# Kernel optimization log

Hardware: AMD Instinct MI355X
Metric: run time of the kernel (lower is better)

## Reference

```python
import jax, jax.numpy as jnp
import numpy as np


def setup_inputs() -> dict:
    key = jax.random.key(0)
    ks = jax.random.split(key, 7)
    B, S, E, N, H = 2, 2048, 1024, 8, 4096
    scale = 0.02
    return {
        "x": jax.random.normal(ks[0], (B, S, E), dtype=jnp.float32),
        "Wr": jax.random.normal(ks[1], (E, N), dtype=jnp.float32) * scale,
        "br": jnp.zeros((N,), dtype=jnp.float32),
        "W1": jax.random.normal(ks[2], (N, E, H), dtype=jnp.float32) * scale,
        "b1": jnp.zeros((N, H), dtype=jnp.float32),
        "W2": jax.random.normal(ks[3], (N, H, E), dtype=jnp.float32) * scale,
        "b2": jnp.zeros((N, E), dtype=jnp.float32),
        "top_k": 2,
    }


def reference(x, Wr, br, W1, b1, W2, b2, top_k):
    # Router: logits [B,S,N], keep top-k, softmax over the kept entries.
    logits = jnp.einsum("bse,en->bsn", x, Wr) + br
    _, idx = jax.lax.top_k(logits, top_k)                      # [B,S,k]
    mask = jax.nn.one_hot(idx, logits.shape[-1], dtype=jnp.bool_).any(-2)  # [B,S,N]
    masked = jnp.where(mask, logits, -jnp.inf)
    weights = jax.nn.softmax(masked, axis=-1)                   # [B,S,N]

    # Dense all-experts FFN (faithful to original): every expert on every token.
    # hid: [B,S,N,H]
    hid = jax.nn.gelu(jnp.einsum("bse,neh->bsnh", x, W1) + b1, approximate=False)
    expert_out = jnp.einsum("bsnh,nhe->bsne", hid, W2) + b2    # [B,S,N,E]
    # dropout is identity in eval mode

    # Weighted combine over experts.
    return jnp.einsum("bsne,bsn->bse", expert_out, weights)
```

## Files before the change

kernel.cpp:

```cpp
#include <hip/hip_runtime.h>
#include <hip/hip_bf16.h>
#include <cmath>
#include <cstdint>


typedef unsigned short u16;
typedef __attribute__((ext_vector_type(8))) short bf16x8;
typedef __attribute__((ext_vector_type(4))) float f32x4;
typedef __attribute__((ext_vector_type(8))) unsigned short us8;
typedef __attribute__((ext_vector_type(4))) unsigned short us4;

#define TOKENS  4096
#define EDIM    1024
#define NEXP    8
#define HDIM    4096
#define MAXROWS 8192
#define ROWPAD  384
#define MAXTILES 40
#define RBLK    1024

#define MFMA16(va, vb, vc) __builtin_amdgcn_mfma_f32_16x16x32_bf16(va, vb, vc, 0, 0, 0)

__device__ __forceinline__ u16 f2bf(float f) {
  __hip_bfloat16 h = __float2bfloat16(f);
  return *reinterpret_cast<u16*>(&h);
}
__device__ __forceinline__ int clampk(int k) {
  return k < 1 ? 1 : (k > 8 ? 8 : k);
}
__device__ __forceinline__ void async16(void* lds, const void* g) {
  __builtin_amdgcn_global_load_lds((const __attribute__((address_space(1))) void*)g,
                                   (__attribute__((address_space(3))) void*)lds,
                                   16, 0, 0);
}
__device__ __forceinline__ float gelu_f(float v) {
  const float z = fabsf(v) * 0.70710678118654752f;
  const float t = __builtin_amdgcn_rcpf(fmaf(0.3275911f, z, 1.0f));
  const float p = t * fmaf(t, fmaf(t, fmaf(t, fmaf(t, 1.061405429f, -1.453152027f),
                                           1.421413741f), -0.284496736f), 0.254829592f);
  float er = 1.0f - p * __expf(-z * z);
  er = copysignf(er, v);
  return 0.5f * v * (1.0f + er);
}

__global__ void router_k(const float* __restrict__ x, const float* __restrict__ Wr,
                         const float* __restrict__ br, const int* __restrict__ topk_p,
                         int* __restrict__ sel_e, float* __restrict__ sel_w,
                         int* __restrict__ sel_lpos, int* __restrict__ hist_blk) {
  __shared__ int wsel[4][8];
  const int blk = blockIdx.x;
  const int tid = threadIdx.x;
  const int wv = tid >> 6, ln = tid & 63;
  const int t = blk * 4 + wv;
  const int k = clampk(topk_p[0]);
  float acc[NEXP];
#pragma unroll
  for (int n = 0; n < NEXP; ++n) acc[n] = 0.f;
  const float* xr = x + (size_t)t * EDIM;
  for (int ei = ln; ei < EDIM; ei += 64) {
    float xv = xr[ei];
    float4 w0 = *(const float4*)(Wr + ei * NEXP);
    float4 w1 = *(const float4*)(Wr + ei * NEXP + 4);
    acc[0] += xv * w0.x; acc[1] += xv * w0.y; acc[2] += xv * w0.z; acc[3] += xv * w0.w;
    acc[4] += xv * w1.x; acc[5] += xv * w1.y; acc[6] += xv * w1.z; acc[7] += xv * w1.w;
  }
#pragma unroll
  for (int s = 32; s > 0; s >>= 1) {
#pragma unroll
    for (int n = 0; n < NEXP; ++n) acc[n] += __shfl_down(acc[n], s);
  }
  if (ln == 0) {
    float logit[NEXP];
#pragma unroll
    for (int n = 0; n < NEXP; ++n) logit[n] = acc[n] + br[n];
    bool used[NEXP];
#pragma unroll
    for (int n = 0; n < NEXP; ++n) used[n] = false;
    int se[NEXP]; float sw[NEXP];
    for (int j = 0; j < k; ++j) {
      int bi = 0; float bv = -INFINITY;
      for (int n = 0; n < NEXP; ++n)
        if (!used[n] && logit[n] > bv) { bv = logit[n]; bi = n; }
      used[bi] = true; se[j] = bi; sw[j] = bv;
    }
    float mx = sw[0], sum = 0.f;
    for (int j = 0; j < k; ++j) { sw[j] = expf(sw[j] - mx); sum += sw[j]; }
    float inv = 1.f / sum;
    for (int j = 0; j < k; ++j) {
      sel_e[t * 8 + j] = se[j];
      sel_w[t * 8 + j] = sw[j] * inv;
      wsel[wv][j] = se[j];
    }
  }
  __syncthreads();
  if (tid == 0) {
    int h[NEXP];
#pragma unroll
    for (int e = 0; e < NEXP; ++e) h[e] = 0;
    for (int w = 0; w < 4; ++w)
      for (int j = 0; j < k; ++j) {
        int e = wsel[w][j];
        sel_lpos[(blk * 4 + w) * 8 + j] = h[e]++;
      }
#pragma unroll
    for (int e = 0; e < NEXP; ++e) hist_blk[blk * NEXP + e] = h[e];
  }
}

__global__ void scan_k(const int* __restrict__ hist_blk, int* __restrict__ counts,
                       int* __restrict__ offsets, int* __restrict__ blk_base,
                       int* __restrict__ tmap) {
  __shared__ int sc[NEXP][257];
  __shared__ int offs[NEXP];
  const int tid = threadIdx.x;
  int h[4][NEXP], part[NEXP];
#pragma unroll
  for (int e = 0; e < NEXP; ++e) part[e] = 0;
#pragma unroll
  for (int r = 0; r < 4; ++r) {
    const int row = tid * 4 + r;
#pragma unroll
    for (int e = 0; e < NEXP; ++e) { h[r][e] = hist_blk[row * NEXP + e]; part[e] += h[r][e]; }
  }
#pragma unroll
  for (int e = 0; e < NEXP; ++e) sc[e][tid] = part[e];
  __syncthreads();
  for (int d = 1; d < 256; d <<= 1) {
    int v[NEXP];
#pragma unroll
    for (int e = 0; e < NEXP; ++e) v[e] = (tid >= d) ? sc[e][tid - d] : 0;
    __syncthreads();
#pragma unroll
    for (int e = 0; e < NEXP; ++e) sc[e][tid] += v[e];
    __syncthreads();
  }
  if (tid == 0) {
    int s = 0;
    for (int e = 0; e < NEXP; ++e) {
      int tot = sc[e][255];
      offsets[e] = s; offs[e] = s; counts[e] = tot; s += tot;
    }
    int nt = 0;
    for (int e = 0; e < NEXP; ++e) {
      int nb = (counts[e] + 255) >> 8;
      for (int b = 0; b < nb && nt < MAXTILES; ++b) tmap[nt++] = (e << 16) | b;
    }
    for (; nt < MAXTILES; ++nt) tmap[nt] = -1;
  }
  __syncthreads();
#pragma unroll
  for (int e = 0; e < NEXP; ++e) {
    int run = offs[e] + sc[e][tid] - part[e];
#pragma unroll
    for (int r = 0; r < 4; ++r) {
      blk_base[(tid * 4 + r) * NEXP + e] = run;
      run += h[r][e];
    }
  }
}

__global__ void finalize_k(const int* __restrict__ sel_e, const int* __restrict__ sel_lpos,
                           const int* __restrict__ blk_base, const int* __restrict__ topk_p,
                           int* __restrict__ sel_pos, int* __restrict__ row_token) {
  const int k = clampk(topk_p[0]);
  const int i = blockIdx.x * 256 + threadIdx.x;
  if (i >= TOKENS * k) return;
  const int t = i / k, j = i - t * k;
  const int e = sel_e[t * 8 + j];
  const int pos = blk_base[(t >> 2) * NEXP + e] + sel_lpos[t * 8 + j];
  sel_pos[t * 8 + j] = pos;
  row_token[pos] = t;
}

__global__ void gather_cast_k(const float* __restrict__ x, const int* __restrict__ row_token,
                              const int* __restrict__ counts, u16* __restrict__ xg,
                              float* __restrict__ Y) {
  __shared__ int tot_s;
  if (threadIdx.x == 0) {
    int t = 0;
#pragma unroll
    for (int e = 0; e < NEXP; ++e) t += counts[e];
    tot_s = t;
  }
  const int row = blockIdx.x;
  const int i = threadIdx.x;
  if (row < MAXROWS) {
    float4 z = {0.f, 0.f, 0.f, 0.f};
    *(float4*)(Y + (size_t)row * EDIM + i * 4) = z;
  }
  __syncthreads();
  u16* dst = xg + (size_t)row * EDIM;
  if (row >= tot_s) {
    us4 z = {0, 0, 0, 0};
    *(us4*)(dst + i * 4) = z;
    return;
  }
  const float* src = x + (size_t)row_token[row] * EDIM;
  float4 v = *(const float4*)(src + i * 4);
  us4 o; o[0] = f2bf(v.x); o[1] = f2bf(v.y); o[2] = f2bf(v.z); o[3] = f2bf(v.w);
  *(us4*)(dst + i * 4) = o;
}

__global__ void transpose_k(const float* __restrict__ W1, const float* __restrict__ W2,
                            u16* __restrict__ W1t, u16* __restrict__ W2t,
                            int full, int h0c) {
  __shared__ __align__(16) u16 T[64][68];
  const int z = blockIdx.z;
  int mat, e, h0;
  if (full) { mat = z < 32 ? 0 : 1; int zz = mat ? z - 32 : z; e = zz >> 2; h0 = (zz & 3) * 1024; }
  else      { mat = z < 8 ? 0 : 1;  e = mat ? z - 8 : z;      h0 = h0c; }
  const size_t oes = full ? (size_t)HDIM * EDIM : (size_t)1024 * 1024;
  const float* in; size_t istride;
  if (mat == 0) { in = W1 + (size_t)e * EDIM * HDIM + h0;            istride = HDIM; }
  else          { in = W2 + (size_t)e * HDIM * EDIM + (size_t)h0 * EDIM; istride = EDIM; }
  const int r0 = blockIdx.y * 64, c0 = blockIdx.x * 64;
  const int tid = threadIdx.x;
#pragma unroll
  for (int it = 0; it < 4; ++it) {
    int cell = it * 256 + tid;
    int rl = cell >> 4, c4 = (cell & 15) * 4;
    float4 v = *(const float4*)(in + (size_t)(r0 + rl) * istride + c0 + c4);
    us4 o; o[0] = f2bf(v.x); o[1] = f2bf(v.y); o[2] = f2bf(v.z); o[3] = f2bf(v.w);
    *(us4*)&T[rl][c4] = o;
  }
  __syncthreads();
#pragma unroll
  for (int it = 0; it < 2; ++it) {
    int cell = it * 256 + tid;
    int cl = cell >> 3, r8 = (cell & 7) * 8;
    us8 o;
#pragma unroll
    for (int j = 0; j < 8; ++j) o[j] = T[r8 + j][cl];
    u16* out;
    if (mat == 0) {
      int orow = (full ? h0 : 0) + c0 + cl;
      out = W1t + (size_t)e * oes + (size_t)orow * 1024 + r0 + r8;
    } else {
      int ost = full ? HDIM : 1024;
      out = W2t + (size_t)e * oes + (size_t)(c0 + cl) * ost + (full ? h0 : 0) + r0 + r8;
    }
    *(us8*)out = o;
  }
}

template <int MODE>
__global__ __launch_bounds__(512, 2) void gemm256_k(
    const u16* __restrict__ A, int astride, int kblocks,
    const u16* __restrict__ Bt, size_t b_estride, int bstride,
    const float* __restrict__ bias, int bias_dim, int bias_col0, int bias_on,
    const int* __restrict__ counts, const int* __restrict__ offsets,
    const int* __restrict__ tmap, int NB,
    u16* __restrict__ hid, int hid_stride, float* __restrict__ Y) {
  __shared__ __align__(16) char lds_s[131072];
  const int bid = blockIdx.x;
  const int by  = blockIdx.y;
  const int tile = bid / NB;
  const int tv = tmap[tile];
  if (tv < 0) return;
  const int n0 = (bid - tile * NB) << 8;
  const int e = tv >> 16;
  const int m0 = (tv & 0xffff) << 8;
  const int cnt = counts[e], off_e = offsets[e];

  const int tid = threadIdx.x;
  const int wv = tid >> 6, ln = tid & 63;
  const int wm = wv >> 2, wn = wv & 3;

  const int trow = tid >> 3;
  const int swz  = (tid & 7) ^ (trow & 7);
  const size_t koff = (size_t)by * kblocks * 64;
  const u16* gA = A + (size_t)(off_e + m0 + trow) * astride + koff + swz * 8;
  const u16* gB = Bt + (size_t)e * b_estride + (size_t)(n0 + trow) * bstride + koff + swz * 8;
  const size_t a64 = (size_t)astride * 64;
  const size_t b64 = (size_t)bstride * 64;
  char* const lA = lds_s + wv * 1024;
  char* const lB = lds_s + 65536 + wv * 1024;

  auto stage = [&](int buf, int kt) {
    const u16* ga = gA + (size_t)kt * 64;
    const u16* gb = gB + (size_t)kt * 64;
    char* la = lA + (buf << 15);
    char* lb = lB + (buf << 15);
#pragma unroll
    for (int h = 0; h < 4; ++h) async16(la + h * 8192, ga + (size_t)h * a64);
#pragma unroll
    for (int h = 0; h < 4; ++h) async16(lb + h * 8192, gb + (size_t)h * b64);
  };

  const int r15 = ln & 15, quad = ln >> 4, rs = r15 & 7;
  const int a_k0 = (wm * 128 + r15) * 128 + (((quad    ) ^ rs) << 4);
  const int a_k1 = (wm * 128 + r15) * 128 + (((quad + 4) ^ rs) << 4);
  const int b_k0 = (wn *  64 + r15) * 128 + (((quad    ) ^ rs) << 4);
  const int b_k1 = (wn *  64 + r15) * 128 + (((quad + 4) ^ rs) << 4);

  f32x4 acc[8][4];
#pragma unroll
  for (int i = 0; i < 8; ++i)
#pragma unroll
    for (int j = 0; j < 4; ++j) acc[i][j] = (f32x4){0.f, 0.f, 0.f, 0.f};

  bf16x8 a0[4], a1[4], b0[4], b1[4];

  stage(0, 0);
  __syncthreads();

  for (int t = 0; t < kblocks; ++t) {
    const int cb = (t & 1) << 15;
    const char* cA = lds_s + cb;
    const char* cB = lds_s + 65536 + cb;

#pragma unroll
    for (int mi = 0; mi < 4; ++mi) {
      a0[mi] = *(const bf16x8*)(cA + a_k0 + mi * 2048);
      a1[mi] = *(const bf16x8*)(cA + a_k1 + mi * 2048);
    }
#pragma unroll
    for (int ni = 0; ni < 4; ++ni) {
      b0[ni] = *(const bf16x8*)(cB + b_k0 + ni * 2048);
      b1[ni] = *(const bf16x8*)(cB + b_k1 + ni * 2048);
    }
    if (t + 1 < kblocks) stage((t & 1) ^ 1, t + 1);

#pragma unroll
    for (int mi = 0; mi < 4; ++mi)
#pragma unroll
      for (int ni = 0; ni < 4; ++ni) {
        acc[mi][ni] = MFMA16(a0[mi], b0[ni], acc[mi][ni]);
        acc[mi][ni] = MFMA16(a1[mi], b1[ni], acc[mi][ni]);
      }

#pragma unroll
    for (int mi = 0; mi < 4; ++mi) {
      a0[mi] = *(const bf16x8*)(cA + a_k0 + (mi + 4) * 2048);
      a1[mi] = *(const bf16x8*)(cA + a_k1 + (mi + 4) * 2048);
    }
#pragma unroll
    for (int mi = 0; mi < 4; ++mi)
#pragma unroll
      for (int ni = 0; ni < 4; ++ni) {
        acc[mi + 4][ni] = MFMA16(a0[mi], b0[ni], acc[mi + 4][ni]);
        acc[mi + 4][ni] = MFMA16(a1[mi], b1[ni], acc[mi + 4][ni]);
      }
    __syncthreads();
  }

  const int col0 = n0 + wn * 64 + r15;
  float bv[4];
#pragma unroll
  for (int ni = 0; ni < 4; ++ni) {
    const float b = bias[(size_t)e * bias_dim + bias_col0 + col0 + ni * 16];
    bv[ni] = (MODE == 0) ? b : ((bias_on && by == 0) ? b : 0.f);
  }
#pragma unroll
  for (int mi = 0; mi < 8; ++mi) {
    const int mb = m0 + wm * 128 + mi * 16 + quad * 4;
#pragma unroll
    for (int ni = 0; ni < 4; ++ni) {
      const int nc = col0 + ni * 16;
#pragma unroll
      for (int r = 0; r < 4; ++r) {
        const int m = mb + r;
        if (m < cnt) {
          const float v = acc[mi][ni][r] + bv[ni];
          if (MODE == 0) {
            hid[(size_t)(off_e + m) * hid_stride + nc] = f2bf(gelu_f(v));
          } else {
            atomicAdd(&Y[(size_t)(off_e + m) * EDIM + nc], v);
          }
        }
      }
    }
  }
}

__global__ void combine_k(const float* __restrict__ Y, const int* __restrict__ sel_pos,
                          const float* __restrict__ sel_w, const int* __restrict__ topk_p,
                          float* __restrict__ out) {
  const int t = blockIdx.x;
  const int tid = threadIdx.x;
  const int k = clampk(topk_p[0]);
  float a0 = 0.f, a1 = 0.f, a2 = 0.f, a3 = 0.f;
  for (int j = 0; j < k; ++j) {
    const float w = sel_w[t * 8 + j];
    const size_t row = (size_t)sel_pos[t * 8 + j];
    const float4 v = *(const float4*)(Y + row * EDIM + tid * 4);
    a0 += w * v.x; a1 += w * v.y; a2 += w * v.z; a3 += w * v.w;
  }
  float4 o; o.x = a0; o.y = a1; o.z = a2; o.w = a3;
  *(float4*)(out + (size_t)t * EDIM + tid * 4) = o;
}

extern "C" void kernel_launch(void* const* d_in, const int* in_sizes, int n_in,
                              void* d_out, int out_size, void* d_ws, size_t ws_size,
                              hipStream_t stream) {
  const float* x   = (const float*)d_in[0];
  const float* Wr  = (const float*)d_in[1];
  const float* br  = (const float*)d_in[2];
  const float* W1  = (const float*)d_in[3];
  const float* b1  = (const float*)d_in[4];
  const float* W2  = (const float*)d_in[5];
  const float* b2  = (const float*)d_in[6];
  const int* topk  = (const int*)d_in[7];
  float* out = (float*)d_out;

  char* ws = (char*)d_ws;
  size_t o = 0;
  auto alloc = [&](size_t bytes) -> char* {
    char* p = ws + o; o += (bytes + 255) & ~(size_t)255; return p;
  };
  int*   counts    = (int*)alloc(NEXP * 4);
  int*   offsets   = (int*)alloc(NEXP * 4);
  int*   tmap      = (int*)alloc(MAXTILES * 4);
  int*   sel_e     = (int*)alloc((size_t)TOKENS * 8 * 4);
  int*   sel_pos   = (int*)alloc((size_t)TOKENS * 8 * 4);
  int*   sel_lpos  = (int*)alloc((size_t)TOKENS * 8 * 4);
  float* sel_w     = (float*)alloc((size_t)TOKENS * 8 * 4);
  int*   row_token = (int*)alloc((size_t)TOKENS * 8 * 4);
  int*   hist_blk  = (int*)alloc((size_t)RBLK * NEXP * 4);
  int*   blk_base  = (int*)alloc((size_t)RBLK * NEXP * 4);
  u16*   xg        = (u16*)alloc((size_t)(MAXROWS + ROWPAD) * EDIM * 2);
  float* Y         = (float*)alloc((size_t)MAXROWS * EDIM * 4);

  const size_t full_need  = ((size_t)NEXP * HDIM * EDIM * 2) * 2
                          + (size_t)(MAXROWS + ROWPAD) * HDIM * 2 + 4096;
  const bool full = (ws_size - o) >= full_need;
  u16 *W1t, *W2t, *hid;
  if (full) {
    W1t = (u16*)alloc((size_t)NEXP * HDIM * EDIM * 2);
    W2t = (u16*)alloc((size_t)NEXP * HDIM * EDIM * 2);
    hid = (u16*)alloc((size_t)(MAXROWS + ROWPAD) * HDIM * 2);
  } else {
    W1t = (u16*)alloc((size_t)NEXP * 1024 * 1024 * 2);
    W2t = (u16*)alloc((size_t)NEXP * 1024 * 1024 * 2);
    hid = (u16*)alloc((size_t)(MAXROWS + ROWPAD) * 1024 * 2);
  }

  router_k<<<dim3(RBLK), dim3(256), 0, stream>>>(x, Wr, br, topk,
                                                 sel_e, sel_w, sel_lpos, hist_blk);
  scan_k<<<dim3(1), dim3(256), 0, stream>>>(hist_blk, counts, offsets, blk_base, tmap);
  finalize_k<<<dim3(TOKENS * 8 / 256), dim3(256), 0, stream>>>(sel_e, sel_lpos, blk_base,
                                                               topk, sel_pos, row_token);
  gather_cast_k<<<dim3(MAXROWS + ROWPAD), dim3(256), 0, stream>>>(x, row_token, counts,
                                                                  xg, Y);

  if (full) {
    transpose_k<<<dim3(16, 16, 64), dim3(256), 0, stream>>>(W1, W2, W1t, W2t, 1, 0);
    gemm256_k<0><<<dim3(MAXTILES * 16, 1), dim3(512), 0, stream>>>(
        xg, EDIM, 16, W1t, (size_t)HDIM * EDIM, EDIM,
        b1, HDIM, 0, 1, counts, offsets, tmap, 16, hid, HDIM, nullptr);
    gemm256_k<1><<<dim3(MAXTILES * 4, 4), dim3(512), 0, stream>>>(
        hid, HDIM, 16, W2t, (size_t)HDIM * EDIM, HDIM,
        b2, EDIM, 0, 1, counts, offsets, tmap, 4, nullptr, 0, Y);
  } else {
    for (int c = 0; c < 4; ++c) {
      const int h0 = c * 1024;
      transpose_k<<<dim3(16, 16, 16), dim3(256), 0, stream>>>(W1, W2, W1t, W2t, 0, h0);
      gemm256_k<0><<<dim3(MAXTILES * 4, 1), dim3(512), 0, stream>>>(
          xg, EDIM, 16, W1t, (size_t)1024 * 1024, 1024,
          b1, HDIM, h0, 1, counts, offsets, tmap, 4, hid, 1024, nullptr);
      gemm256_k<1><<<dim3(MAXTILES * 4, 1), dim3(512), 0, stream>>>(
          hid, 1024, 16, W2t, (size_t)1024 * 1024, 1024,
          b2, EDIM, 0, (c == 0) ? 1 : 0, counts, offsets, tmap, 4, nullptr, 0, Y);
    }
  }
  combine_k<<<dim3(TOKENS), dim3(256), 0, stream>>>(Y, sel_pos, sel_w, topk, out);
}
```

Before: 661.5 us.

## Shrink grouped GEMM tiles to 128x128 and drop split-K atomics

Replaces the 256x256, 512-thread double-buffered grouped GEMM with a 128x128, 256-thread single-buffered kernel, and routes tokens in 128-row expert tiles to cut padding waste. The second GEMM now runs the full K in one block and writes Y directly, so there are no split-K atomics and no zero-fill of Y in the gather kernel. The costs are lower per-block data reuse, loss of the load/compute overlap from double buffering, and more blocks plus syncs per K step.

New measurement: 567.8 us. 14.2% less time.

```diff
diff --git a/kernel.cpp b/kernel.cpp
--- a/kernel.cpp
+++ b/kernel.cpp
@@ -15,8 +15,8 @@
 #define NEXP    8
 #define HDIM    4096
 #define MAXROWS 8192
-#define ROWPAD  384
-#define MAXTILES 40
+#define ROWPAD  128
+#define MAXTILES 72
 #define RBLK    1024
 
 #define MFMA16(va, vb, vc) __builtin_amdgcn_mfma_f32_16x16x32_bf16(va, vb, vc, 0, 0, 0)
@@ -142,7 +142,7 @@
     }
     int nt = 0;
     for (int e = 0; e < NEXP; ++e) {
-      int nb = (counts[e] + 255) >> 8;
+      int nb = (counts[e] + 127) >> 7;
       for (int b = 0; b < nb && nt < MAXTILES; ++b) tmap[nt++] = (e << 16) | b;
     }
     for (; nt < MAXTILES; ++nt) tmap[nt] = -1;
@@ -173,8 +173,7 @@
 }
 
 __global__ void gather_cast_k(const float* __restrict__ x, const int* __restrict__ row_token,
-                              const int* __restrict__ counts, u16* __restrict__ xg,
-                              float* __restrict__ Y) {
+                              const int* __restrict__ counts, u16* __restrict__ xg) {
   __shared__ int tot_s;
   if (threadIdx.x == 0) {
     int t = 0;
@@ -182,14 +181,10 @@
     for (int e = 0; e < NEXP; ++e) t += counts[e];
     tot_s = t;
   }
+  __syncthreads();
   const int row = blockIdx.x;
+  u16* dst = xg + (size_t)row * EDIM;
   const int i = threadIdx.x;
-  if (row < MAXROWS) {
-    float4 z = {0.f, 0.f, 0.f, 0.f};
-    *(float4*)(Y + (size_t)row * EDIM + i * 4) = z;
-  }
-  __syncthreads();
-  u16* dst = xg + (size_t)row * EDIM;
   if (row >= tot_s) {
     us4 z = {0, 0, 0, 0};
     *(us4*)(dst + i * 4) = z;
@@ -244,83 +239,71 @@
 }
 
 template <int MODE>
-__global__ __launch_bounds__(512, 2) void gemm256_k(
+__global__ __launch_bounds__(256, 3) void gemm_k(
     const u16* __restrict__ A, int astride, int kblocks,
     const u16* __restrict__ Bt, size_t b_estride, int bstride,
     const float* __restrict__ bias, int bias_dim, int bias_col0, int bias_on,
     const int* __restrict__ counts, const int* __restrict__ offsets,
     const int* __restrict__ tmap, int NB,
-    u16* __restrict__ hid, int hid_stride, float* __restrict__ Y) {
-  __shared__ __align__(16) char lds_s[131072];
+    u16* __restrict__ hid, int hid_stride, float* __restrict__ Y, int accum) {
+  __shared__ __align__(16) u16 As[128 * 64];
+  __shared__ __align__(16) u16 Bs[128 * 64];
   const int bid = blockIdx.x;
-  const int by  = blockIdx.y;
   const int tile = bid / NB;
   const int tv = tmap[tile];
   if (tv < 0) return;
-  const int n0 = (bid - tile * NB) << 8;
+  const int n0 = (bid - tile * NB) << 7;
   const int e = tv >> 16;
-  const int m0 = (tv & 0xffff) << 8;
+  const int m0 = (tv & 0xffff) << 7;
   const int cnt = counts[e], off_e = offsets[e];
 
   const int tid = threadIdx.x;
   const int wv = tid >> 6, ln = tid & 63;
-  const int wm = wv >> 2, wn = wv & 3;
+  const int wm = wv >> 1, wn = wv & 1;
 
   const int trow = tid >> 3;
   const int swz  = (tid & 7) ^ (trow & 7);
-  const size_t koff = (size_t)by * kblocks * 64;
-  const u16* gA = A + (size_t)(off_e + m0 + trow) * astride + koff + swz * 8;
-  const u16* gB = Bt + (size_t)e * b_estride + (size_t)(n0 + trow) * bstride + koff + swz * 8;
-  const size_t a64 = (size_t)astride * 64;
-  const size_t b64 = (size_t)bstride * 64;
-  char* const lA = lds_s + wv * 1024;
-  char* const lB = lds_s + 65536 + wv * 1024;
-
-  auto stage = [&](int buf, int kt) {
-    const u16* ga = gA + (size_t)kt * 64;
-    const u16* gb = gB + (size_t)kt * 64;
-    char* la = lA + (buf << 15);
-    char* lb = lB + (buf << 15);
-#pragma unroll
-    for (int h = 0; h < 4; ++h) async16(la + h * 8192, ga + (size_t)h * a64);
-#pragma unroll
-    for (int h = 0; h < 4; ++h) async16(lb + h * 8192, gb + (size_t)h * b64);
-  };
+  const u16* gA = A + (size_t)(off_e + m0 + trow) * astride + swz * 8;
+  const u16* gB = Bt + (size_t)e * b_estride + (size_t)(n0 + trow) * bstride + swz * 8;
+  const size_t a32 = (size_t)astride * 32;
+  const size_t b32 = (size_t)bstride * 32;
+  u16* const lA = As + wv * 512;
+  u16* const lB = Bs + wv * 512;
 
   const int r15 = ln & 15, quad = ln >> 4, rs = r15 & 7;
-  const int a_k0 = (wm * 128 + r15) * 128 + (((quad    ) ^ rs) << 4);
-  const int a_k1 = (wm * 128 + r15) * 128 + (((quad + 4) ^ rs) << 4);
-  const int b_k0 = (wn *  64 + r15) * 128 + (((quad    ) ^ rs) << 4);
-  const int b_k1 = (wn *  64 + r15) * 128 + (((quad + 4) ^ rs) << 4);
-
-  f32x4 acc[8][4];
-#pragma unroll
-  for (int i = 0; i < 8; ++i)
+  const int arow = (wm * 64 + r15) * 64;
+  const int brow = (wn * 64 + r15) * 64;
+  const int s0 = (quad ^ rs) * 8;
+  const int s1 = ((quad + 4) ^ rs) * 8;
+
+  f32x4 acc[4][4];
+#pragma unroll
+  for (int i = 0; i < 4; ++i)
 #pragma unroll
     for (int j = 0; j < 4; ++j) acc[i][j] = (f32x4){0.f, 0.f, 0.f, 0.f};
 
-  bf16x8 a0[4], a1[4], b0[4], b1[4];
-
-  stage(0, 0);
-  __syncthreads();
-
-  for (int t = 0; t < kblocks; ++t) {
-    const int cb = (t & 1) << 15;
-    const char* cA = lds_s + cb;
-    const char* cB = lds_s + 65536 + cb;
-
+  for (int kb = 0; kb < kblocks; ++kb) {
+    const int k0 = kb * 64;
+    __syncthreads();
+    const u16* ga = gA + k0;
+    const u16* gb = gB + k0;
+#pragma unroll
+    for (int h = 0; h < 4; ++h) async16(lA + h * 2048, ga + (size_t)h * a32);
+#pragma unroll
+    for (int h = 0; h < 4; ++h) async16(lB + h * 2048, gb + (size_t)h * b32);
+    __syncthreads();
+
+    bf16x8 a0[4], a1[4], b0[4], b1[4];
 #pragma unroll
     for (int mi = 0; mi < 4; ++mi) {
-      a0[mi] = *(const bf16x8*)(cA + a_k0 + mi * 2048);
-      a1[mi] = *(const bf16x8*)(cA + a_k1 + mi * 2048);
+      a0[mi] = *(const bf16x8*)(As + arow + mi * 1024 + s0);
+      a1[mi] = *(const bf16x8*)(As + arow + mi * 1024 + s1);
     }
 #pragma unroll
     for (int ni = 0; ni < 4; ++ni) {
-      b0[ni] = *(const bf16x8*)(cB + b_k0 + ni * 2048);
-      b1[ni] = *(const bf16x8*)(cB + b_k1 + ni * 2048);
-    }
-    if (t + 1 < kblocks) stage((t & 1) ^ 1, t + 1);
-
+      b0[ni] = *(const bf16x8*)(Bs + brow + ni * 1024 + s0);
+      b1[ni] = *(const bf16x8*)(Bs + brow + ni * 1024 + s1);
+    }
 #pragma unroll
     for (int mi = 0; mi < 4; ++mi)
 #pragma unroll
@@ -328,20 +311,6 @@
         acc[mi][ni] = MFMA16(a0[mi], b0[ni], acc[mi][ni]);
         acc[mi][ni] = MFMA16(a1[mi], b1[ni], acc[mi][ni]);
       }
-
-#pragma unroll
-    for (int mi = 0; mi < 4; ++mi) {
-      a0[mi] = *(const bf16x8*)(cA + a_k0 + (mi + 4) * 2048);
-      a1[mi] = *(const bf16x8*)(cA + a_k1 + (mi + 4) * 2048);
-    }
-#pragma unroll
-    for (int mi = 0; mi < 4; ++mi)
-#pragma unroll
-      for (int ni = 0; ni < 4; ++ni) {
-        acc[mi + 4][ni] = MFMA16(a0[mi], b0[ni], acc[mi + 4][ni]);
-        acc[mi + 4][ni] = MFMA16(a1[mi], b1[ni], acc[mi + 4][ni]);
-      }
-    __syncthreads();
   }
 
   const int col0 = n0 + wn * 64 + r15;
@@ -349,11 +318,11 @@
 #pragma unroll
   for (int ni = 0; ni < 4; ++ni) {
     const float b = bias[(size_t)e * bias_dim + bias_col0 + col0 + ni * 16];
-    bv[ni] = (MODE == 0) ? b : ((bias_on && by == 0) ? b : 0.f);
-  }
-#pragma unroll
-  for (int mi = 0; mi < 8; ++mi) {
-    const int mb = m0 + wm * 128 + mi * 16 + quad * 4;
+    bv[ni] = (MODE == 0) ? b : (bias_on ? b : 0.f);
+  }
+#pragma unroll
+  for (int mi = 0; mi < 4; ++mi) {
+    const int mb = m0 + wm * 64 + mi * 16 + quad * 4;
 #pragma unroll
     for (int ni = 0; ni < 4; ++ni) {
       const int nc = col0 + ni * 16;
@@ -365,7 +334,8 @@
           if (MODE == 0) {
             hid[(size_t)(off_e + m) * hid_stride + nc] = f2bf(gelu_f(v));
           } else {
-            atomicAdd(&Y[(size_t)(off_e + m) * EDIM + nc], v);
+            size_t yi = (size_t)(off_e + m) * EDIM + nc;
+            Y[yi] = accum ? (Y[yi] + v) : v;
           }
         }
       }
@@ -440,27 +410,27 @@
   scan_k<<<dim3(1), dim3(256), 0, stream>>>(hist_blk, counts, offsets, blk_base, tmap);
   finalize_k<<<dim3(TOKENS * 8 / 256), dim3(256), 0, stream>>>(sel_e, sel_lpos, blk_base,
                                                                topk, sel_pos, row_token);
-  gather_cast_k<<<dim3(MAXROWS + ROWPAD), dim3(256), 0, stream>>>(x, row_token, counts,
-                                                                  xg, Y);
+  gather_cast_k<<<dim3(MAXROWS + ROWPAD), dim3(256), 0, stream>>>(x, row_token, counts, xg);
 
   if (full) {
     transpose_k<<<dim3(16, 16, 64), dim3(256), 0, stream>>>(W1, W2, W1t, W2t, 1, 0);
-    gemm256_k<0><<<dim3(MAXTILES * 16, 1), dim3(512), 0, stream>>>(
-        xg, EDIM, 16, W1t, (size_t)HDIM * EDIM, EDIM,
-        b1, HDIM, 0, 1, counts, offsets, tmap, 16, hid, HDIM, nullptr);
-    gemm256_k<1><<<dim3(MAXTILES * 4, 4), dim3(512), 0, stream>>>(
-        hid, HDIM, 16, W2t, (size_t)HDIM * EDIM, HDIM,
-        b2, EDIM, 0, 1, counts, offsets, tmap, 4, nullptr, 0, Y);
+    gemm_k<0><<<dim3(MAXTILES * 32), dim3(256), 0, stream>>>(
+        xg, EDIM, 16, W1t, (size_t)HDIM * EDIM, 1024,
+        b1, HDIM, 0, 1, counts, offsets, tmap, 32, hid, HDIM, nullptr, 0);
+    gemm_k<1><<<dim3(MAXTILES * 8), dim3(256), 0, stream>>>(
+        hid, HDIM, 64, W2t, (size_t)HDIM * EDIM, HDIM,
+        b2, EDIM, 0, 1, counts, offsets, tmap, 8, nullptr, 0, Y, 0);
   } else {
     for (int c = 0; c < 4; ++c) {
       const int h0 = c * 1024;
       transpose_k<<<dim3(16, 16, 16), dim3(256), 0, stream>>>(W1, W2, W1t, W2t, 0, h0);
-      gemm256_k<0><<<dim3(MAXTILES * 4, 1), dim3(512), 0, stream>>>(
+      gemm_k<0><<<dim3(MAXTILES * 8), dim3(256), 0, stream>>>(
           xg, EDIM, 16, W1t, (size_t)1024 * 1024, 1024,
-          b1, HDIM, h0, 1, counts, offsets, tmap, 4, hid, 1024, nullptr);
-      gemm256_k<1><<<dim3(MAXTILES * 4, 1), dim3(512), 0, stream>>>(
+          b1, HDIM, h0, 1, counts, offsets, tmap, 8, hid, 1024, nullptr, 0);
+      gemm_k<1><<<dim3(MAXTILES * 8), dim3(256), 0, stream>>>(
           hid, 1024, 16, W2t, (size_t)1024 * 1024, 1024,
-          b2, EDIM, 0, (c == 0) ? 1 : 0, counts, offsets, tmap, 4, nullptr, 0, Y);
+          b2, EDIM, 0, (c == 0) ? 1 : 0, counts, offsets, tmap, 8, nullptr, 0, Y,
+          (c == 0) ? 0 : 1);
     }
   }
   combine_k<<<dim3(TOKENS), dim3(256), 0, stream>>>(Y, sel_pos, sel_w, topk, out);
```
